# Kernel optimization log

Measured on AMD Instinct MI355X. Metric: run time of the kernel, lower is better.

Reference implementation:

```python
import jax, jax.numpy as jnp
import numpy as np

B, N, C = 8, 4096, 896
OUT = 896


def setup_inputs() -> dict:
    key = jax.random.key(0)
    ks = jax.random.split(key, 8)
    s = 0.02
    return {
        "x_": jax.random.normal(ks[0], (B, N, C), dtype=jnp.float32),
        "Wq": jax.random.normal(ks[1], (C, C), dtype=jnp.float32) * s,
        "Wk": jax.random.normal(ks[2], (C, C), dtype=jnp.float32) * s,
        "Wv": jax.random.normal(ks[3], (C, C), dtype=jnp.float32) * s,
        "Wp": jax.random.normal(ks[4], (C, C), dtype=jnp.float32) * s,
        "bp": jnp.zeros((C,), dtype=jnp.float32),
        "Wf1": jax.random.normal(ks[5], (C, C), dtype=jnp.float32) * s,
        "bf1": jnp.zeros((C,), dtype=jnp.float32),
        "Wf2": jax.random.normal(ks[6], (C, OUT), dtype=jnp.float32) * s,
        "bf2": jnp.zeros((OUT,), dtype=jnp.float32),
    }


def reference(x_, Wq, Wk, Wv, Wp, bp, Wf1, bf1, Wf2, bf2):
    scale = x_.shape[-1] ** (-0.5)  # q_dim ** -0.5
    q = jnp.einsum('bnc,cd->bnd', x_, Wq)
    k = jnp.einsum('bnc,cd->bnd', x_, Wk)
    v = jnp.einsum('bnc,cd->bnd', x_, Wv)
    attn = jnp.einsum('bnd,bmd->bnm', q, k) * scale  # [B,N,N]
    attn = jax.nn.softmax(attn, axis=-1)
    x = jnp.einsum('bnm,bmd->bnd', attn, v)
    x = jnp.einsum('bnd,de->bne', x, Wp) + bp + x_
    x = jnp.mean(x, axis=1)  # [B,C] (mean pool over tokens)
    h = jax.nn.relu(jnp.einsum('bc,cd->bd', x, Wf1) + bf1)
    out = jnp.einsum('bd,de->be', h, Wf2) + bf2  # dropout p=0.0 -> identity
    return out
```

## Files before the change

kernel.cpp:

```cpp
#include <hip/hip_runtime.h>
#include <cmath>

typedef unsigned short u16;
typedef __attribute__((ext_vector_type(8))) short v8s;
typedef __attribute__((ext_vector_type(4))) short v4s;
typedef __attribute__((ext_vector_type(4))) float f32x4;

#define NBATCH 8
#define SEQ 4096
#define CH 896
#define NC ((size_t)SEQ * CH)
#define NN ((size_t)SEQ * SEQ)

__device__ __forceinline__ float b2f(u16 u) {
  unsigned v = ((unsigned)u) << 16;
  return __builtin_bit_cast(float, v);
}
__device__ __forceinline__ u16 f2b(float f) {
  unsigned u = __builtin_bit_cast(unsigned, f);
  u += 0x7FFFu + ((u >> 16) & 1u);
  return (u16)(u >> 16);
}

__device__ __forceinline__ f32x4 mfma16(v8s a, v8s b, f32x4 c) {
  asm("v_mfma_f32_16x16x32_bf16 %0, %1, %2, %0" : "+v"(c) : "v"(a), "v"(b));
  return c;
}

__device__ __forceinline__ void gload16(const u16* g, u16* l) {
  __builtin_amdgcn_global_load_lds(
      (const __attribute__((address_space(1))) unsigned int*)g,
      (__attribute__((address_space(3))) unsigned int*)l, 16, 0, 0);
}

__launch_bounds__(256)
__global__ void cvt_k(const float* __restrict__ in, u16* __restrict__ out)
{
  const size_t i = ((size_t)blockIdx.x * 256 + threadIdx.x) * 8;
  const float4 a = *(const float4*)(in + i);
  const float4 b = *(const float4*)(in + i + 4);
  union { v8s v; u16 u[8]; } o;
  o.u[0] = f2b(a.x); o.u[1] = f2b(a.y); o.u[2] = f2b(a.z); o.u[3] = f2b(a.w);
  o.u[4] = f2b(b.x); o.u[5] = f2b(b.y); o.u[6] = f2b(b.z); o.u[7] = f2b(b.w);
  *(v8s*)(out + i) = o.v;
}

template<int MODE>
__launch_bounds__(256)
__global__ void gemm_k(const u16* __restrict__ A, const u16* __restrict__ B,
                       u16* __restrict__ outp, float* __restrict__ lsum, float scale,
                       size_t az, size_t bz, size_t oz, int lz)
{
  __shared__ __align__(16) u16 As[128 * 32];
  __shared__ __align__(16) u16 Bs[128 * 32];
  const int z = blockIdx.z;
  A += (size_t)z * az; B += (size_t)z * bz; outp += (size_t)z * oz;
  if constexpr (MODE == 1) lsum += z * lz;
  const int tid  = threadIdx.x;
  const int lane = tid & 63;
  const int wv   = tid >> 6;
  const int wr   = (wv >> 1) * 64;
  const int wc   = (wv & 1) * 64;
  const int row0 = blockIdx.x * 128;
  const int col0 = blockIdx.y * 128;
  const int srow = tid >> 2;
  const int sk   = (tid & 3) * 8;
  const u16* ag = A + (size_t)(row0 + srow) * CH + sk;
  const u16* bg = B + (size_t)(col0 + srow) * CH + sk;
  u16* asd = As + tid * 8;
  u16* bsd = Bs + tid * 8;

  f32x4 acc[4][4];
  #pragma unroll
  for (int i = 0; i < 4; i++)
    #pragma unroll
    for (int j = 0; j < 4; j++)
      acc[i][j] = f32x4{0.f, 0.f, 0.f, 0.f};

  const int lo = lane & 15, hi = lane >> 4;
  const int kk = hi * 8;

  for (int k0 = 0; k0 < CH; k0 += 32) {
    __syncthreads();
    gload16(ag + k0, asd);
    gload16(ag + (size_t)64 * CH + k0, asd + 64 * 32);
    gload16(bg + k0, bsd);
    gload16(bg + (size_t)64 * CH + k0, bsd + 64 * 32);
    __syncthreads();
    v8s af[4], bf[4];
    #pragma unroll
    for (int f = 0; f < 4; f++) af[f] = *(const v8s*)(As + (wr + lo + f * 16) * 32 + kk);
    #pragma unroll
    for (int f = 0; f < 4; f++) bf[f] = *(const v8s*)(Bs + (wc + lo + f * 16) * 32 + kk);
    #pragma unroll
    for (int i = 0; i < 4; i++)
      #pragma unroll
      for (int j = 0; j < 4; j++)
        acc[i][j] = mfma16(af[i], bf[j], acc[i][j]);
  }
  __builtin_amdgcn_sched_barrier(0);
  asm volatile("s_nop 7\ns_nop 7\ns_nop 7");
  __builtin_amdgcn_sched_barrier(0);

  if constexpr (MODE == 0) {
    #pragma unroll
    for (int i = 0; i < 4; i++)
      #pragma unroll
      for (int j = 0; j < 4; j++) {
        const int col = col0 + wc + j * 16 + lo;
        #pragma unroll
        for (int r = 0; r < 4; r++) {
          const int row = row0 + wr + i * 16 + hi * 4 + r;
          outp[(size_t)row * CH + col] = f2b(acc[i][j][r]);
        }
      }
  } else if constexpr (MODE == 1) {
    float rsum[4][4];
    #pragma unroll
    for (int i = 0; i < 4; i++)
      #pragma unroll
      for (int r = 0; r < 4; r++) rsum[i][r] = 0.f;
    #pragma unroll
    for (int i = 0; i < 4; i++)
      #pragma unroll
      for (int j = 0; j < 4; j++) {
        const int col = col0 + wc + j * 16 + lo;
        #pragma unroll
        for (int r = 0; r < 4; r++) {
          const float e = __expf(acc[i][j][r]);
          rsum[i][r] += e;
          const int row = row0 + wr + i * 16 + hi * 4 + r;
          outp[(size_t)row * SEQ + col] = f2b(e);
        }
      }
    #pragma unroll
    for (int msk = 1; msk < 16; msk <<= 1)
      #pragma unroll
      for (int i = 0; i < 4; i++)
        #pragma unroll
        for (int r = 0; r < 4; r++)
          rsum[i][r] += __shfl_xor(rsum[i][r], msk, 64);
    if (lo == 0) {
      #pragma unroll
      for (int i = 0; i < 4; i++)
        #pragma unroll
        for (int r = 0; r < 4; r++)
          atomicAdd(&lsum[row0 + wr + i * 16 + hi * 4 + r], rsum[i][r]);
    }
  } else {
    #pragma unroll
    for (int i = 0; i < 4; i++)
      #pragma unroll
      for (int j = 0; j < 4; j++) {
        const int col = col0 + wc + j * 16 + lo;
        #pragma unroll
        for (int r = 0; r < 4; r++) {
          const int row = row0 + wr + i * 16 + hi * 4 + r;
          outp[(size_t)col * CH + row] = f2b(acc[i][j][r] * scale);
        }
      }
  }
}

__launch_bounds__(256)
__global__ void w_k(const u16* __restrict__ E, const float* __restrict__ l,
                    float* __restrict__ w, size_t ez, int lz)
{
  __shared__ float rl[128];
  const int t = threadIdx.x;
  const int z = blockIdx.z;
  E += (size_t)z * ez; l += z * lz; w += z * lz;
  const int n0 = blockIdx.x * 128;
  const int m0 = (blockIdx.y * 256 + t) * 4;
  if (t < 128) rl[t] = 1.0f / l[n0 + t];
  __syncthreads();
  float a0 = 0.f, a1 = 0.f, a2 = 0.f, a3 = 0.f;
  const u16* ep = E + (size_t)n0 * SEQ + m0;
  #pragma unroll 4
  for (int n = 0; n < 128; n++) {
    union { v4s v; u16 u[4]; } e;
    e.v = *(const v4s*)(ep + (size_t)n * SEQ);
    const float r = rl[n];
    a0 = fmaf(b2f(e.u[0]), r, a0);
    a1 = fmaf(b2f(e.u[1]), r, a1);
    a2 = fmaf(b2f(e.u[2]), r, a2);
    a3 = fmaf(b2f(e.u[3]), r, a3);
  }
  atomicAdd(&w[m0 + 0], a0);
  atomicAdd(&w[m0 + 1], a1);
  atomicAdd(&w[m0 + 2], a2);
  atomicAdd(&w[m0 + 3], a3);
}

__launch_bounds__(256)
__global__ void sx_k(const float* __restrict__ x, const float* __restrict__ w,
                     float* __restrict__ s, float* __restrict__ mx)
{
  const int b  = blockIdx.x;
  const int c  = blockIdx.y * 256 + threadIdx.x;
  const int m0 = blockIdx.z * 256;
  if (c >= CH) return;
  const float* xb = x + (size_t)b * NC;
  const float* wb = w + b * SEQ;
  float sw = 0.f, sxv = 0.f;
  for (int m = m0; m < m0 + 256; m++) {
    const float xv = xb[(size_t)m * CH + c];
    sw  = fmaf(wb[m], xv, sw);
    sxv += xv;
  }
  const float inv = 1.0f / (float)SEQ;
  atomicAdd(&s[b * CH + c], sw * inv);
  atomicAdd(&mx[b * CH + c], sxv * inv);
}

template<int EPI>
__launch_bounds__(256)
__global__ void gemv_k(const float* __restrict__ in, const float* __restrict__ W,
                       const float* __restrict__ bias, const float* __restrict__ mx,
                       float* __restrict__ outacc)
{
  __shared__ float vin[128];
  const int t  = threadIdx.x;
  const int b  = blockIdx.y;
  const int n0 = blockIdx.x * 128;
  const int k0 = blockIdx.z * 128;
  if (t < 128) {
    float v = in[b * CH + k0 + t];
    if constexpr (EPI == 1) v = v + bias[k0 + t] + mx[b * CH + k0 + t];
    if constexpr (EPI == 2) v = fmaxf(v + bias[k0 + t], 0.f);
    vin[t] = v;
  }
  __syncthreads();
  const int col = n0 + (t & 127);
  const int kh  = (t >> 7) * 64;
  const float* wp = W + (size_t)(k0 + kh) * CH + col;
  float acc = 0.f;
  #pragma unroll 8
  for (int i = 0; i < 64; i++)
    acc = fmaf(vin[kh + i], wp[(size_t)i * CH], acc);
  atomicAdd(&outacc[b * CH + col], acc);
}

__global__ void initout_k(const float* __restrict__ bf2, float* __restrict__ out)
{
  out[blockIdx.x * CH + threadIdx.x] = bf2[threadIdx.x];
}

extern "C" void kernel_launch(void* const* d_in, const int* in_sizes, int n_in,
                              void* d_out, int out_size, void* d_ws, size_t ws_size,
                              hipStream_t stream)
{
  (void)in_sizes; (void)n_in; (void)out_size;
  const float* x   = (const float*)d_in[0];
  const float* Wq  = (const float*)d_in[1];
  const float* Wk  = (const float*)d_in[2];
  const float* Wv  = (const float*)d_in[3];
  const float* Wp  = (const float*)d_in[4];
  const float* bp  = (const float*)d_in[5];
  const float* Wf1 = (const float*)d_in[6];
  const float* bf1 = (const float*)d_in[7];
  const float* Wf2 = (const float*)d_in[8];
  const float* bf2 = (const float*)d_in[9];
  float* out = (float*)d_out;

  char* ws = (char*)d_ws;
  float* l_  = (float*)(ws + 0);
  float* w_  = (float*)(ws + 131072);
  float* s_  = (float*)(ws + 262144);
  float* mx_ = (float*)(ws + 290816);
  float* t1_ = (float*)(ws + 319488);
  float* t2_ = (float*)(ws + 348160);
  float* h_  = (float*)(ws + 376832);
  u16* wqb = (u16*)(ws + 405504);
  u16* wkb = (u16*)(ws + 2011136);
  u16* mt  = (u16*)(ws + 3616768);
  u16* xb  = (u16*)(ws + 5222400);

  hipMemsetAsync(d_ws, 0, 405504, stream);
  initout_k<<<8, 896, 0, stream>>>(bf2, out);

  cvt_k<<<392, 256, 0, stream>>>(Wq, wqb);
  cvt_k<<<392, 256, 0, stream>>>(Wk, wkb);
  const float scale = 1.0f / sqrtf((float)CH);
  gemm_k<2><<<dim3(7, 7), 256, 0, stream>>>(wqb, wkb, mt, nullptr, scale, 0, 0, 0, 0);

  if (ws_size >= 391098368ULL) {
    u16* yb = (u16*)(ws + 63942656ULL);
    u16* eb = (u16*)(ws + 122662912ULL);
    cvt_k<<<14336, 256, 0, stream>>>(x, xb);
    gemm_k<0><<<dim3(256, 7), 256, 0, stream>>>(xb, mt, yb, nullptr, 1.f, 0, 0, 0, 0);
    gemm_k<1><<<dim3(32, 32, NBATCH), 256, 0, stream>>>(yb, xb, eb, l_, 1.f,
                                                        NC, NC, NN, SEQ);
    w_k<<<dim3(32, 4, NBATCH), 256, 0, stream>>>(eb, l_, w_, NN, SEQ);
  } else {
    u16* yb = (u16*)(ws + 12562432);
    u16* eb = (u16*)(ws + 19902464);
    const size_t ecap = ws_size > 19902464ULL ? ws_size - 19902464ULL : 0;
    int R = (int)(ecap / ((size_t)SEQ * 2) / 128) * 128;
    if (R > SEQ) R = SEQ;
    if (R < 128) R = 128;
    for (int b = 0; b < NBATCH; b++) {
      cvt_k<<<1792, 256, 0, stream>>>(x + (size_t)b * NC, xb);
      gemm_k<0><<<dim3(32, 7), 256, 0, stream>>>(xb, mt, yb, nullptr, 1.f, 0, 0, 0, 0);
      for (int n0 = 0; n0 < SEQ; n0 += R) {
        const int rows = (SEQ - n0) < R ? (SEQ - n0) : R;
        gemm_k<1><<<dim3(rows / 128, 32), 256, 0, stream>>>(
            yb + (size_t)n0 * CH, xb, eb, l_ + b * SEQ + n0, 1.f, 0, 0, 0, 0);
        w_k<<<dim3(rows / 128, 4), 256, 0, stream>>>(
            eb, l_ + b * SEQ + n0, w_ + b * SEQ, 0, 0);
      }
    }
  }

  sx_k<<<dim3(8, 4, 16), 256, 0, stream>>>(x, w_, s_, mx_);

  const dim3 gv(7, 8, 7);
  gemv_k<0><<<gv, 256, 0, stream>>>(s_,  Wv,  nullptr, nullptr, t1_);
  gemv_k<0><<<gv, 256, 0, stream>>>(t1_, Wp,  nullptr, nullptr, t2_);
  gemv_k<1><<<gv, 256, 0, stream>>>(t2_, Wf1, bp,      mx_,     h_);
  gemv_k<2><<<gv, 256, 0, stream>>>(h_,  Wf2, bf1,     nullptr, out);
}
```

Baseline: 706.4 us.

## Add 256x256-tile score GEMM with 4-stage LDS pipeline and fused exp/rowsum

Replaces the batched 128x128 score GEMM (Y·Xᵀ plus exp and row sums) with a new 512-thread kernel that computes 256x256 output tiles. It uses a 4-deep direct-to-LDS load pipeline with explicit vmcnt waits and barriers. The larger tile raises arithmetic intensity and halves operand re-reads, and the deeper prefetch aims to hide global latency behind MFMA work. In exchange it uses 128 KB of LDS per block and 128 accumulator registers per lane, which limits occupancy. The epilogue writes scattered bf16 stores and issues per-row atomicAdds.

```diff
diff --git a/kernel.cpp b/kernel.cpp
--- a/kernel.cpp
+++ b/kernel.cpp
@@ -27,10 +27,10 @@
   return c;
 }
 
-__device__ __forceinline__ void gload16(const u16* g, u16* l) {
+__device__ __forceinline__ void gload16(const u16* g, const u16* l) {
   __builtin_amdgcn_global_load_lds(
       (const __attribute__((address_space(1))) unsigned int*)g,
-      (__attribute__((address_space(3))) unsigned int*)l, 16, 0, 0);
+      (__attribute__((address_space(3))) unsigned int*)(u16*)l, 16, 0, 0);
 }
 
 __launch_bounds__(256)
@@ -43,6 +43,109 @@
   o.u[0] = f2b(a.x); o.u[1] = f2b(a.y); o.u[2] = f2b(a.z); o.u[3] = f2b(a.w);
   o.u[4] = f2b(b.x); o.u[5] = f2b(b.y); o.u[6] = f2b(b.z); o.u[7] = f2b(b.w);
   *(v8s*)(out + i) = o.v;
+}
+
+__launch_bounds__(512, 2)
+__global__ void sgemm_k(const u16* __restrict__ A, const u16* __restrict__ B,
+                        u16* __restrict__ E, float* __restrict__ lsum)
+{
+  __shared__ __align__(16) u16 sh[65536];
+  const int z = blockIdx.z;
+  A += (size_t)z * NC; B += (size_t)z * NC;
+  E += (size_t)z * NN; lsum += z * SEQ;
+
+  const int tid  = threadIdx.x;
+  const int lane = tid & 63;
+  const int wid  = tid >> 6;
+  const int wm   = wid >> 2;
+  const int wn   = wid & 3;
+  const int lo   = lane & 15, hi = lane >> 4;
+  const int row0 = blockIdx.x * 256;
+  const int col0 = blockIdx.y * 256;
+
+  const int arow  = wm * 128 + wn * 32;
+  const int bh    = wn >> 1;
+  const int brow2 = bh * 128 + ((wm << 1) | (wn & 1)) * 32;
+  const u16* gA0 = A + (size_t)(row0 + arow  + (lane >> 2)) * CH + (lane & 3) * 8;
+  const u16* gB0 = B + (size_t)(col0 + brow2 + (lane >> 2)) * CH + (lane & 3) * 8;
+  const int aL = arow * 32;
+  const int bL = 8192 + brow2 * 32;
+
+  f32x4 acc[8][4];
+  #pragma unroll
+  for (int f = 0; f < 8; f++)
+    #pragma unroll
+    for (int j = 0; j < 4; j++)
+      acc[f][j] = f32x4{0.f, 0.f, 0.f, 0.f};
+
+  #define STAGE(t) do {                                               \
+    const int bo_ = ((t) & 3) * 16384;                                \
+    const size_t ko_ = (size_t)(t) * 32;                              \
+    gload16(gA0 + ko_,            sh + bo_ + aL);                     \
+    gload16(gA0 + 16 * CH + ko_,  sh + bo_ + aL + 512);               \
+    gload16(gB0 + ko_,            sh + bo_ + bL);                     \
+    gload16(gB0 + 16 * CH + ko_,  sh + bo_ + bL + 512);               \
+  } while (0)
+
+  STAGE(0); STAGE(1); STAGE(2);
+  __builtin_amdgcn_sched_barrier(0);
+  asm volatile("s_waitcnt vmcnt(8)" ::: "memory");
+  __builtin_amdgcn_s_barrier();
+  __builtin_amdgcn_sched_barrier(0);
+
+  #pragma unroll 1
+  for (int t = 0; t < 28; ++t) {
+    if (t < 25) STAGE(t + 3);
+    const int bo = (t & 3) * 16384;
+    v8s bfrag[4];
+    #pragma unroll
+    for (int j = 0; j < 4; j++)
+      bfrag[j] = *(const v8s*)(sh + bo + 8192 + (wn * 64 + j * 16 + lo) * 32 + hi * 8);
+    #pragma unroll
+    for (int f = 0; f < 8; f++) {
+      const v8s afrag = *(const v8s*)(sh + bo + (wm * 128 + f * 16 + lo) * 32 + hi * 8);
+      #pragma unroll
+      for (int j = 0; j < 4; j++)
+        acc[f][j] = mfma16(afrag, bfrag[j], acc[f][j]);
+    }
+    __builtin_amdgcn_sched_barrier(0);
+    if (t < 25)       asm volatile("s_waitcnt vmcnt(8)" ::: "memory");
+    else if (t == 25) asm volatile("s_waitcnt vmcnt(4)" ::: "memory");
+    else              asm volatile("s_waitcnt vmcnt(0)" ::: "memory");
+    __builtin_amdgcn_s_barrier();
+    __builtin_amdgcn_sched_barrier(0);
+  }
+  #undef STAGE
+
+  __builtin_amdgcn_sched_barrier(0);
+  asm volatile("s_nop 7\ns_nop 7\ns_nop 7");
+  __builtin_amdgcn_sched_barrier(0);
+
+  #pragma unroll
+  for (int f = 0; f < 8; f++) {
+    float rs[4] = {0.f, 0.f, 0.f, 0.f};
+    #pragma unroll
+    for (int j = 0; j < 4; j++) {
+      const int col = col0 + wn * 64 + j * 16 + lo;
+      #pragma unroll
+      for (int r = 0; r < 4; r++) {
+        const float e = __expf(acc[f][j][r]);
+        rs[r] += e;
+        const int row = row0 + wm * 128 + f * 16 + hi * 4 + r;
+        E[(size_t)row * SEQ + col] = f2b(e);
+      }
+    }
+    #pragma unroll
+    for (int msk = 1; msk < 16; msk <<= 1)
+      #pragma unroll
+      for (int r = 0; r < 4; r++)
+        rs[r] += __shfl_xor(rs[r], msk, 64);
+    if (lo == 0) {
+      #pragma unroll
+      for (int r = 0; r < 4; r++)
+        atomicAdd(&lsum[row0 + wm * 128 + f * 16 + hi * 4 + r], rs[r]);
+    }
+  }
 }
 
 template<int MODE>
@@ -289,8 +392,7 @@
     u16* eb = (u16*)(ws + 122662912ULL);
     cvt_k<<<14336, 256, 0, stream>>>(x, xb);
     gemm_k<0><<<dim3(256, 7), 256, 0, stream>>>(xb, mt, yb, nullptr, 1.f, 0, 0, 0, 0);
-    gemm_k<1><<<dim3(32, 32, NBATCH), 256, 0, stream>>>(yb, xb, eb, l_, 1.f,
-                                                        NC, NC, NN, SEQ);
+    sgemm_k<<<dim3(16, 16, NBATCH), 512, 0, stream>>>(yb, xb, eb, l_);
     w_k<<<dim3(32, 4, NBATCH), 256, 0, stream>>>(eb, l_, w_, NN, SEQ);
   } else {
     u16* yb = (u16*)(ws + 12562432);
```

Result: slower. 729.9 us (+3.3%).
